# Kernel tuning notes

Measured on AMD Instinct MI355X. Metric: run time of the kernel, lower is better.

The kernel has to match this reference:

```python
import jax, jax.numpy as jnp
import numpy as np

REG_MAX = 16
NUM_CLASSES = 80
STRIDES = (8, 16, 32)
FEAT_SIZES = ((80, 80), (40, 40), (20, 20))
CLS_DIM = 256
REG_DIM = 256
B = 16


def setup_inputs() -> dict:
    key = jax.random.key(0)
    ks = jax.random.split(key, 32)
    inp = {}
    i = 0
    for l, (H, W) in enumerate(FEAT_SIZES):
        inp[f"cls_feat{l}"] = jax.random.normal(ks[i], (B, CLS_DIM, H, W), jnp.float32); i += 1
        inp[f"reg_feat{l}"] = jax.random.normal(ks[i], (B, REG_DIM, H, W), jnp.float32); i += 1
    bias_init = -float(np.log((1.0 - 0.01) / 0.01))
    for l in range(3):
        inp[f"obj_w{l}"] = jax.random.normal(ks[i], (1, REG_DIM), jnp.float32) * 0.02; i += 1
        inp[f"obj_b{l}"] = jnp.full((1,), bias_init, jnp.float32)
        inp[f"cls_w{l}"] = jax.random.normal(ks[i], (NUM_CLASSES, CLS_DIM), jnp.float32) * 0.02; i += 1
        inp[f"cls_b{l}"] = jnp.full((NUM_CLASSES,), bias_init, jnp.float32)
        inp[f"reg_w{l}"] = jax.random.normal(ks[i], (4 * REG_MAX, REG_DIM), jnp.float32) * 0.02; i += 1
        inp[f"reg_b{l}"] = jnp.ones((4 * REG_MAX,), jnp.float32)
    return inp


def _anchors(H, W, stride):
    ay, ax = jnp.meshgrid(jnp.arange(H, dtype=jnp.float32), jnp.arange(W, dtype=jnp.float32), indexing="ij")
    a = jnp.stack([ax, ay], axis=-1).reshape(-1, 2)  # [HW, 2] (x, y)
    return (a + 0.5) * stride


def _level(cls_feat, reg_feat, obj_w, obj_b, cls_w, cls_b, reg_w, reg_b, stride):
    Bb, _, H, W = cls_feat.shape
    M = H * W
    # 1x1 convs as channel contractions; output in [B, H, W, O] then flatten to [B, M, O]
    obj = (jnp.einsum("bchw,oc->bhwo", reg_feat, obj_w) + obj_b).reshape(Bb, M, 1)
    cls = (jnp.einsum("bchw,oc->bhwo", cls_feat, cls_w) + cls_b).reshape(Bb, M, NUM_CLASSES)
    reg = (jnp.einsum("bchw,oc->bhwo", reg_feat, reg_w) + reg_b).reshape(Bb, M, 4 * REG_MAX)
    # DFL decode: softmax over bins, expectation with proj = linspace(0, reg_max, reg_max)
    proj = jnp.linspace(0.0, float(REG_MAX), REG_MAX)
    dist = jax.nn.softmax(reg.reshape(Bb, M, 4, REG_MAX), axis=-1)
    reg_d = jnp.einsum("bmfr,r->bmf", dist, proj)  # [B, M, 4] (l, t, r, b)
    anchors = _anchors(H, W, stride)  # [M, 2]
    x1y1 = anchors[None] - reg_d[..., :2] * stride
    x2y2 = anchors[None] + reg_d[..., 2:] * stride
    box = jnp.concatenate([x1y1, x2y2], axis=-1)  # [B, M, 4]
    return jnp.concatenate([obj, cls, reg, box], axis=-1)  # [B, M, 1+80+64+4]


def reference(cls_feat0, cls_feat1, cls_feat2, reg_feat0, reg_feat1, reg_feat2,
              obj_w0, obj_b0, cls_w0, cls_b0, reg_w0, reg_b0,
              obj_w1, obj_b1, cls_w1, cls_b1, reg_w1, reg_b1,
              obj_w2, obj_b2, cls_w2, cls_b2, reg_w2, reg_b2):
    lvl0 = _level(cls_feat0, reg_feat0, obj_w0, obj_b0, cls_w0, cls_b0, reg_w0, reg_b0, STRIDES[0])
    lvl1 = _level(cls_feat1, reg_feat1, obj_w1, obj_b1, cls_w1, cls_b1, reg_w1, reg_b1, STRIDES[1])
    lvl2 = _level(cls_feat2, reg_feat2, obj_w2, obj_b2, cls_w2, cls_b2, reg_w2, reg_b2, STRIDES[2])
    # concat anchors along M: [B, 8400, 149]
    return jnp.concatenate([lvl0, lvl1, lvl2], axis=1)
```

## Files before the change

kernel.cpp:

```cpp
#include <hip/hip_runtime.h>
#include <stdint.h>

typedef __attribute__((ext_vector_type(4))) float f32x4;
typedef __attribute__((ext_vector_type(8))) short s16x8;

struct Params {
  const float* cls_feat[3];
  const float* reg_feat[3];
  const float* obj_w[3];
  const float* obj_b[3];
  const float* cls_w[3];
  const float* cls_b[3];
  const float* reg_w[3];
  const float* reg_b[3];
  float* out;
};

__device__ __forceinline__ unsigned short f2bf(float f) {
  unsigned int u = __builtin_bit_cast(unsigned int, f);
  u = (u + 0x7FFFu + ((u >> 16) & 1u)) >> 16;
  return (unsigned short)u;
}

__global__ __launch_bounds__(320, 5) void head_kernel(Params p) {
  const int tid  = threadIdx.x;
  const int lane = tid & 63;
  const int wave = tid >> 6;
  const int quad = lane >> 4;
  const int col  = lane & 15;
  const bool is_cls = (blockIdx.y == 0);

  int bx = blockIdx.x;
  int b  = bx / 105;
  int t  = bx - b * 105;
  int level, tloc;
  if (t < 80)       { level = 0; tloc = t; }
  else if (t < 100) { level = 1; tloc = t - 80; }
  else              { level = 2; tloc = t - 100; }

  const int   LW_[3]   = {80, 40, 20};
  const int   LM_[3]   = {6400, 1600, 400};
  const float LS_[3]   = {8.f, 16.f, 32.f};
  const int   LOFF_[3] = {0, 6400, 8000};

  const int   Mlvl = LM_[level];
  const int   Moff = LOFF_[level];
  const float strd = LS_[level];
  const int   m0   = tloc * 80;

  __shared__ __align__(16) short lds_feat[80 * 256];

  const f32x4 vzero = {0.f, 0.f, 0.f, 0.f};

  const int orow = wave * 16 + col;
  const float* wptr;
  if (is_cls)          wptr = p.cls_w[level] + orow * 256;
  else if (orow < 64)  wptr = p.reg_w[level] + orow * 256;
  else if (orow == 64) wptr = p.obj_w[level];
  else                 wptr = nullptr;

  f32x4 wv[16];
  #pragma unroll
  for (int s = 0; s < 8; ++s) {
    if (wptr) {
      const f32x4* wp = (const f32x4*)(wptr + s * 32 + quad * 8);
      wv[2 * s]     = wp[0];
      wv[2 * s + 1] = wp[1];
    } else {
      wv[2 * s]     = vzero;
      wv[2 * s + 1] = vzero;
    }
  }

  f32x4 bias = vzero;
  {
    const int o0 = wave * 16 + quad * 4;
    if (is_cls)        bias = *(const f32x4*)(p.cls_b[level] + o0);
    else if (o0 < 64)  bias = *(const f32x4*)(p.reg_b[level] + o0);
    else if (o0 == 64) bias[0] = p.obj_b[level][0];
  }

  const int mloc = tid % 80;
  const int cb0  = tid / 80;
  const float* featp = (is_cls ? p.cls_feat[level] : p.reg_feat[level])
                       + (size_t)b * 256 * (size_t)Mlvl + m0 + mloc;

  float f[2][8];
  #pragma unroll
  for (int j = 0; j < 8; ++j) f[0][j] = featp[(size_t)(cb0 * 8 + j) * Mlvl];

  s16x8 afrag[8];
  #pragma unroll
  for (int s = 0; s < 8; ++s) {
    s16x8 a;
    #pragma unroll
    for (int j = 0; j < 4; ++j) {
      a[j]     = (short)f2bf(wv[2 * s][j]);
      a[4 + j] = (short)f2bf(wv[2 * s + 1][j]);
    }
    afrag[s] = a;
  }

  const int swz = mloc & 7;
  #pragma unroll
  for (int i = 0; i < 8; ++i) {
    if (i < 7) {
      const int cbn = cb0 + 4 * (i + 1);
      #pragma unroll
      for (int j = 0; j < 8; ++j)
        f[(i + 1) & 1][j] = featp[(size_t)(cbn * 8 + j) * Mlvl];
    }
    const int cb = cb0 + 4 * i;
    s16x8 h;
    #pragma unroll
    for (int j = 0; j < 8; ++j) h[j] = (short)f2bf(f[i & 1][j]);
    *(s16x8*)&lds_feat[mloc * 256 + ((cb ^ swz) << 3)] = h;
  }

  __syncthreads();

  f32x4 acc[5];
  #pragma unroll
  for (int mf = 0; mf < 5; ++mf) acc[mf] = vzero;
  #pragma unroll
  for (int mf = 0; mf < 5; ++mf) {
    const int row = mf * 16 + col;
    const short* base = &lds_feat[row * 256];
    const int rswz = row & 7;
    #pragma unroll
    for (int s = 0; s < 8; ++s) {
      s16x8 bfrag = *(const s16x8*)(base + (((s * 4 + quad) ^ rswz) << 3));
      acc[mf] = __builtin_amdgcn_mfma_f32_16x16x32_bf16(afrag[s], bfrag, acc[mf], 0, 0, 0);
    }
  }

  const size_t outbase = (size_t)b * 8400 + Moff + m0;
  float* out = p.out;

  if (is_cls) {
    #pragma unroll
    for (int mf = 0; mf < 5; ++mf) {
      const int m = mf * 16 + col;
      f32x4 v = acc[mf] + bias;
      float* dst = out + (outbase + m) * 149 + 1 + wave * 16 + quad * 4;
      __builtin_memcpy(dst, &v, 16);
    }
    return;
  }

  float* g_lds = (float*)lds_feat;
  __syncthreads();

  if (wave < 4) {
    const float projscale = 16.f / 15.f;
    #pragma unroll
    for (int mf = 0; mf < 5; ++mf) {
      const int m = mf * 16 + col;
      f32x4 v = acc[mf] + bias;
      float* dst = out + (outbase + m) * 149 + 81 + wave * 16 + quad * 4;
      __builtin_memcpy(dst, &v, 16);
      float mx = fmaxf(fmaxf(v[0], v[1]), fmaxf(v[2], v[3]));
      mx = fmaxf(mx, __shfl_xor(mx, 16, 64));
      mx = fmaxf(mx, __shfl_xor(mx, 32, 64));
      const float e0 = __expf(v[0] - mx), e1 = __expf(v[1] - mx);
      const float e2 = __expf(v[2] - mx), e3 = __expf(v[3] - mx);
      float sden = e0 + e1 + e2 + e3;
      const float q4 = (float)(quad * 4);
      float n = q4 * e0 + (q4 + 1.f) * e1 + (q4 + 2.f) * e2 + (q4 + 3.f) * e3;
      sden += __shfl_xor(sden, 16, 64); sden += __shfl_xor(sden, 32, 64);
      n    += __shfl_xor(n, 16, 64);    n    += __shfl_xor(n, 32, 64);
      if (quad == 0) g_lds[wave * 80 + m] = projscale * n / sden;
    }
  } else {
    #pragma unroll
    for (int mf = 0; mf < 5; ++mf) {
      const int m = mf * 16 + col;
      if (quad == 0) out[(outbase + m) * 149] = acc[mf][0] + bias[0];
    }
  }

  __syncthreads();

  if (wave == 4) {
    #pragma unroll
    for (int it = 0; it < 2; ++it) {
      const int m = it * 64 + lane;
      if (m < 80) {
        const float g0 = g_lds[m], g1 = g_lds[80 + m];
        const float g2 = g_lds[160 + m], g3 = g_lds[240 + m];
        const int mg = m0 + m;
        int hh;
        if (level == 0)      hh = mg / 80;
        else if (level == 1) hh = mg / 40;
        else                 hh = mg / 20;
        const int ww = mg - hh * LW_[level];
        const float ax = (ww + 0.5f) * strd;
        const float ay = (hh + 0.5f) * strd;
        f32x4 bv;
        bv[0] = ax - g0 * strd; bv[1] = ay - g1 * strd;
        bv[2] = ax + g2 * strd; bv[3] = ay + g3 * strd;
        float* dst = out + (outbase + m) * 149 + 145;
        __builtin_memcpy(dst, &bv, 16);
      }
    }
  }
}

extern "C" void kernel_launch(void* const* d_in, const int* in_sizes, int n_in,
                              void* d_out, int out_size, void* d_ws, size_t ws_size,
                              hipStream_t stream) {
  (void)in_sizes; (void)n_in; (void)out_size; (void)d_ws; (void)ws_size;
  Params p;
  p.cls_feat[0] = (const float*)d_in[0];
  p.reg_feat[0] = (const float*)d_in[1];
  p.cls_feat[1] = (const float*)d_in[2];
  p.reg_feat[1] = (const float*)d_in[3];
  p.cls_feat[2] = (const float*)d_in[4];
  p.reg_feat[2] = (const float*)d_in[5];
  for (int l = 0; l < 3; ++l) {
    const int base = 6 + l * 6;
    p.obj_w[l] = (const float*)d_in[base + 0];
    p.obj_b[l] = (const float*)d_in[base + 1];
    p.cls_w[l] = (const float*)d_in[base + 2];
    p.cls_b[l] = (const float*)d_in[base + 3];
    p.reg_w[l] = (const float*)d_in[base + 4];
    p.reg_b[l] = (const float*)d_in[base + 5];
  }
  p.out = (float*)d_out;

  dim3 grid(16 * 105, 2);
  dim3 block(320);
  hipLaunchKernelGGL(head_kernel, grid, block, 0, stream, p);
}
```

Measured before the change: 358.7 us.

## Load feature tiles as float4 vectors and interleave weight/feature staging

Feature loading changes from scalar per-channel loads (one spatial position per thread) to 16-byte vector loads covering four spatial positions across four channels per thread. The values are transposed into LDS with a new XOR swizzle key to avoid bank conflicts. Weight loads and bf16 conversion are software-pipelined alongside the feature staging so global latency overlaps conversion work. The intent is to cut global load instruction count and improve coalescing, in exchange for more live registers and narrower 8-byte LDS writes.

```diff
diff --git a/kernel.cpp b/kernel.cpp
--- a/kernel.cpp
+++ b/kernel.cpp
@@ -3,6 +3,7 @@
 
 typedef __attribute__((ext_vector_type(4))) float f32x4;
 typedef __attribute__((ext_vector_type(8))) short s16x8;
+typedef __attribute__((ext_vector_type(4))) short s16x4;
 
 struct Params {
   const float* cls_feat[3];
@@ -22,6 +23,30 @@
   return (unsigned short)u;
 }
 
+__device__ __forceinline__ s16x8 cvt8(f32x4 a, f32x4 b, bool valid) {
+  s16x8 r;
+  #pragma unroll
+  for (int j = 0; j < 4; ++j) {
+    r[j]     = valid ? (short)f2bf(a[j]) : (short)0;
+    r[4 + j] = valid ? (short)f2bf(b[j]) : (short)0;
+  }
+  return r;
+}
+
+__device__ __forceinline__ void stage4(short* lds, int mq, int tq, int i,
+                                       f32x4 L0, f32x4 L1, f32x4 L2, f32x4 L3) {
+  #pragma unroll
+  for (int j = 0; j < 4; ++j) {
+    const int m   = mq * 4 + j;
+    const int key = ((m >> 2) ^ m) & 7;
+    const int swc = (tq >> 1) ^ key;
+    s16x4 h;
+    h[0] = (short)f2bf(L0[j]); h[1] = (short)f2bf(L1[j]);
+    h[2] = (short)f2bf(L2[j]); h[3] = (short)f2bf(L3[j]);
+    *(s16x4*)&lds[m * 256 + i * 64 + swc * 8 + (tq & 1) * 4] = h;
+  }
+}
+
 __global__ __launch_bounds__(320, 5) void head_kernel(Params p) {
   const int tid  = threadIdx.x;
   const int lane = tid & 63;
@@ -39,9 +64,9 @@
   else              { level = 2; tloc = t - 100; }
 
   const int   LW_[3]   = {80, 40, 20};
-  const int   LM_[3]   = {6400, 1600, 400};
   const float LS_[3]   = {8.f, 16.f, 32.f};
   const int   LOFF_[3] = {0, 6400, 8000};
+  const int   LM_[3]   = {6400, 1600, 400};
 
   const int   Mlvl = LM_[level];
   const int   Moff = LOFF_[level];
@@ -51,6 +76,12 @@
   __shared__ __align__(16) short lds_feat[80 * 256];
 
   const f32x4 vzero = {0.f, 0.f, 0.f, 0.f};
+
+  const int tq = tid / 20;
+  const int mq = tid - tq * 20;
+
+  const float* featp = (is_cls ? p.cls_feat[level] : p.reg_feat[level])
+                       + (size_t)b * 256 * (size_t)Mlvl + m0 + mq * 4;
 
   const int orow = wave * 16 + col;
   const float* wptr;
@@ -58,19 +89,19 @@
   else if (orow < 64)  wptr = p.reg_w[level] + orow * 256;
   else if (orow == 64) wptr = p.obj_w[level];
   else                 wptr = nullptr;
-
-  f32x4 wv[16];
-  #pragma unroll
-  for (int s = 0; s < 8; ++s) {
-    if (wptr) {
-      const f32x4* wp = (const f32x4*)(wptr + s * 32 + quad * 8);
-      wv[2 * s]     = wp[0];
-      wv[2 * s + 1] = wp[1];
-    } else {
-      wv[2 * s]     = vzero;
-      wv[2 * s + 1] = vzero;
-    }
-  }
+  const bool  wvalid = (wptr != nullptr);
+  const float* wq    = (wvalid ? wptr : p.obj_w[level]) + quad * 8;
+
+  #define WLD(s, h) (*(const f32x4*)(wq + (s) * 32 + (h) * 4))
+  #define FLD(i, c) (*(const f32x4*)(featp + (size_t)((i) * 64 + tq * 4 + (c)) * (size_t)Mlvl))
+
+  s16x8 afrag[8];
+  f32x4 wa, wb, wc, wd;
+  f32x4 A0, A1, A2, A3, B0, B1, B2, B3;
+
+  wa = WLD(0, 0); wb = WLD(0, 1); wc = WLD(1, 0); wd = WLD(1, 1);
+  A0 = FLD(0, 0); A1 = FLD(0, 1); A2 = FLD(0, 2); A3 = FLD(0, 3);
+  B0 = FLD(1, 0); B1 = FLD(1, 1); B2 = FLD(1, 2); B3 = FLD(1, 3);
 
   f32x4 bias = vzero;
   {
@@ -80,42 +111,19 @@
     else if (o0 == 64) bias[0] = p.obj_b[level][0];
   }
 
-  const int mloc = tid % 80;
-  const int cb0  = tid / 80;
-  const float* featp = (is_cls ? p.cls_feat[level] : p.reg_feat[level])
-                       + (size_t)b * 256 * (size_t)Mlvl + m0 + mloc;
-
-  float f[2][8];
-  #pragma unroll
-  for (int j = 0; j < 8; ++j) f[0][j] = featp[(size_t)(cb0 * 8 + j) * Mlvl];
-
-  s16x8 afrag[8];
-  #pragma unroll
-  for (int s = 0; s < 8; ++s) {
-    s16x8 a;
-    #pragma unroll
-    for (int j = 0; j < 4; ++j) {
-      a[j]     = (short)f2bf(wv[2 * s][j]);
-      a[4 + j] = (short)f2bf(wv[2 * s + 1][j]);
-    }
-    afrag[s] = a;
-  }
-
-  const int swz = mloc & 7;
-  #pragma unroll
-  for (int i = 0; i < 8; ++i) {
-    if (i < 7) {
-      const int cbn = cb0 + 4 * (i + 1);
-      #pragma unroll
-      for (int j = 0; j < 8; ++j)
-        f[(i + 1) & 1][j] = featp[(size_t)(cbn * 8 + j) * Mlvl];
-    }
-    const int cb = cb0 + 4 * i;
-    s16x8 h;
-    #pragma unroll
-    for (int j = 0; j < 8; ++j) h[j] = (short)f2bf(f[i & 1][j]);
-    *(s16x8*)&lds_feat[mloc * 256 + ((cb ^ swz) << 3)] = h;
-  }
+  afrag[0] = cvt8(wa, wb, wvalid); afrag[1] = cvt8(wc, wd, wvalid);
+  wa = WLD(2, 0); wb = WLD(2, 1); wc = WLD(3, 0); wd = WLD(3, 1);
+  stage4(lds_feat, mq, tq, 0, A0, A1, A2, A3);
+  A0 = FLD(2, 0); A1 = FLD(2, 1); A2 = FLD(2, 2); A3 = FLD(2, 3);
+  afrag[2] = cvt8(wa, wb, wvalid); afrag[3] = cvt8(wc, wd, wvalid);
+  wa = WLD(4, 0); wb = WLD(4, 1); wc = WLD(5, 0); wd = WLD(5, 1);
+  stage4(lds_feat, mq, tq, 1, B0, B1, B2, B3);
+  B0 = FLD(3, 0); B1 = FLD(3, 1); B2 = FLD(3, 2); B3 = FLD(3, 3);
+  afrag[4] = cvt8(wa, wb, wvalid); afrag[5] = cvt8(wc, wd, wvalid);
+  wa = WLD(6, 0); wb = WLD(6, 1); wc = WLD(7, 0); wd = WLD(7, 1);
+  stage4(lds_feat, mq, tq, 2, A0, A1, A2, A3);
+  afrag[6] = cvt8(wa, wb, wvalid); afrag[7] = cvt8(wc, wd, wvalid);
+  stage4(lds_feat, mq, tq, 3, B0, B1, B2, B3);
 
   __syncthreads();
 
@@ -124,12 +132,14 @@
   for (int mf = 0; mf < 5; ++mf) acc[mf] = vzero;
   #pragma unroll
   for (int mf = 0; mf < 5; ++mf) {
-    const int row = mf * 16 + col;
+    const int row  = mf * 16 + col;
+    const int rkey = ((row >> 2) ^ row) & 7;
     const short* base = &lds_feat[row * 256];
-    const int rswz = row & 7;
     #pragma unroll
     for (int s = 0; s < 8; ++s) {
-      s16x8 bfrag = *(const s16x8*)(base + (((s * 4 + quad) ^ rswz) << 3));
+      const int c16 = 4 * s + quad;
+      const int sw  = (c16 & ~7) | ((c16 & 7) ^ rkey);
+      s16x8 bfrag = *(const s16x8*)(base + sw * 8);
       acc[mf] = __builtin_amdgcn_mfma_f32_16x16x32_bf16(afrag[s], bfrag, acc[mf], 0, 0, 0);
     }
   }
```

Measured after the change: 359.2 us. About the same (+0.1%).

## Stage features via global_load_lds with 64-anchor tiles and fused cls/reg phases

Applied to the files above, without the earlier changes.

Each block now handles 64 anchors instead of 80 and processes both the cls and the reg/obj branch in sequence, replacing the two-block-per-tile grid. Feature channels are loaded with direct global-to-LDS loads into an fp32 tile in two 128-channel halves, using a rotated layout. The bf16 conversion now happens when the B fragments are read back from LDS. The aim is to cut register-staged loads and launch overhead and to improve load issue. In exchange the LDS reads become scalar strided loads with conversion inside the MFMA loop, and each block adds extra syncs.

```diff
diff --git a/kernel.cpp b/kernel.cpp
--- a/kernel.cpp
+++ b/kernel.cpp
@@ -22,172 +22,172 @@
   return (unsigned short)u;
 }
 
+__device__ __forceinline__ s16x8 cvt8(f32x4 a, f32x4 b, bool ok) {
+  s16x8 r;
+  #pragma unroll
+  for (int j = 0; j < 4; ++j) {
+    r[j]     = ok ? (short)f2bf(a[j]) : (short)0;
+    r[4 + j] = ok ? (short)f2bf(b[j]) : (short)0;
+  }
+  return r;
+}
+
+__device__ __forceinline__ void gload_lds4(const float* g, float* l) {
+  __builtin_amdgcn_global_load_lds(
+      (const __attribute__((address_space(1))) unsigned int*)g,
+      (__attribute__((address_space(3))) unsigned int*)l, 4, 0, 0);
+}
+
 __global__ __launch_bounds__(320, 5) void head_kernel(Params p) {
   const int tid  = threadIdx.x;
   const int lane = tid & 63;
   const int wave = tid >> 6;
   const int quad = lane >> 4;
   const int col  = lane & 15;
-  const bool is_cls = (blockIdx.y == 0);
 
   int bx = blockIdx.x;
-  int b  = bx / 105;
-  int t  = bx - b * 105;
+  int b  = bx / 132;
+  int t  = bx - b * 132;
   int level, tloc;
-  if (t < 80)       { level = 0; tloc = t; }
-  else if (t < 100) { level = 1; tloc = t - 80; }
-  else              { level = 2; tloc = t - 100; }
+  if (t < 100)      { level = 0; tloc = t; }
+  else if (t < 125) { level = 1; tloc = t - 100; }
+  else              { level = 2; tloc = t - 125; }
 
   const int   LW_[3]   = {80, 40, 20};
-  const int   LM_[3]   = {6400, 1600, 400};
   const float LS_[3]   = {8.f, 16.f, 32.f};
   const int   LOFF_[3] = {0, 6400, 8000};
+  const int   LM_[3]   = {6400, 1600, 400};
 
   const int   Mlvl = LM_[level];
   const int   Moff = LOFF_[level];
   const float strd = LS_[level];
-  const int   m0   = tloc * 80;
-
-  __shared__ __align__(16) short lds_feat[80 * 256];
-
-  const f32x4 vzero = {0.f, 0.f, 0.f, 0.f};
-
-  const int orow = wave * 16 + col;
-  const float* wptr;
-  if (is_cls)          wptr = p.cls_w[level] + orow * 256;
-  else if (orow < 64)  wptr = p.reg_w[level] + orow * 256;
-  else if (orow == 64) wptr = p.obj_w[level];
-  else                 wptr = nullptr;
-
-  f32x4 wv[16];
-  #pragma unroll
-  for (int s = 0; s < 8; ++s) {
-    if (wptr) {
-      const f32x4* wp = (const f32x4*)(wptr + s * 32 + quad * 8);
-      wv[2 * s]     = wp[0];
-      wv[2 * s + 1] = wp[1];
-    } else {
-      wv[2 * s]     = vzero;
-      wv[2 * s + 1] = vzero;
-    }
-  }
-
-  f32x4 bias = vzero;
-  {
-    const int o0 = wave * 16 + quad * 4;
+  const int   m0   = tloc * 64;
+  int valid = Mlvl - m0; if (valid > 64) valid = 64;
+
+  __shared__ __align__(16) float lds_f[128 * 64];
+
+  const size_t outbase = (size_t)b * 8400 + Moff + m0;
+  float* out = p.out;
+  const int orow    = wave * 16 + col;
+  const int o0      = wave * 16 + quad * 4;
+  const int rotbase = col + quad * 8;
+
+  for (int ph = 0; ph < 2; ++ph) {
+    const bool is_cls = (ph == 0);
+    const float* featp = (is_cls ? p.cls_feat[level] : p.reg_feat[level])
+                         + (size_t)b * 256 * (size_t)Mlvl + m0;
+
+    const float* wptr;
+    bool wvalid = true;
+    if (is_cls)          wptr = p.cls_w[level] + orow * 256;
+    else if (orow < 64)  wptr = p.reg_w[level] + orow * 256;
+    else if (orow == 64) wptr = p.obj_w[level];
+    else               { wptr = p.obj_w[level]; wvalid = false; }
+    const float* wq = wptr + quad * 8;
+
+    f32x4 bias = {0.f, 0.f, 0.f, 0.f};
     if (is_cls)        bias = *(const f32x4*)(p.cls_b[level] + o0);
     else if (o0 < 64)  bias = *(const f32x4*)(p.reg_b[level] + o0);
     else if (o0 == 64) bias[0] = p.obj_b[level][0];
-  }
-
-  const int mloc = tid % 80;
-  const int cb0  = tid / 80;
-  const float* featp = (is_cls ? p.cls_feat[level] : p.reg_feat[level])
-                       + (size_t)b * 256 * (size_t)Mlvl + m0 + mloc;
-
-  float f[2][8];
-  #pragma unroll
-  for (int j = 0; j < 8; ++j) f[0][j] = featp[(size_t)(cb0 * 8 + j) * Mlvl];
-
-  s16x8 afrag[8];
-  #pragma unroll
-  for (int s = 0; s < 8; ++s) {
-    s16x8 a;
+
+    f32x4 acc[4];
     #pragma unroll
-    for (int j = 0; j < 4; ++j) {
-      a[j]     = (short)f2bf(wv[2 * s][j]);
-      a[4 + j] = (short)f2bf(wv[2 * s + 1][j]);
+    for (int mf = 0; mf < 4; ++mf) acc[mf] = (f32x4){0.f, 0.f, 0.f, 0.f};
+
+    #pragma unroll
+    for (int h = 0; h < 2; ++h) {
+      __syncthreads();
+
+      const float* wqh = wq + h * 128;
+      f32x4 w0a = *(const f32x4*)(wqh + 0);
+      f32x4 w0b = *(const f32x4*)(wqh + 4);
+      f32x4 w1a = *(const f32x4*)(wqh + 32);
+      f32x4 w1b = *(const f32x4*)(wqh + 36);
+
+      for (int r = wave; r < 128; r += 5) {
+        const int rot = ((r >> 3) & 3) << 3;
+        int mi = (lane - rot) & 63;
+        if (mi >= valid) mi = valid - 1;
+        gload_lds4(featp + (size_t)(h * 128 + r) * (size_t)Mlvl + mi,
+                   &lds_f[r * 64]);
+      }
+
+      s16x8 af0 = cvt8(w0a, w0b, wvalid);
+      s16x8 af1 = cvt8(w1a, w1b, wvalid);
+      f32x4 w2a = *(const f32x4*)(wqh + 64);
+      f32x4 w2b = *(const f32x4*)(wqh + 68);
+      f32x4 w3a = *(const f32x4*)(wqh + 96);
+      f32x4 w3b = *(const f32x4*)(wqh + 100);
+
+      __syncthreads();
+
+      s16x8 af2 = cvt8(w2a, w2b, wvalid);
+      s16x8 af3 = cvt8(w3a, w3b, wvalid);
+      s16x8 afr[4] = {af0, af1, af2, af3};
+
+      #pragma unroll
+      for (int mf = 0; mf < 4; ++mf) {
+        const int rotm = (rotbase + mf * 16) & 63;
+        #pragma unroll
+        for (int s = 0; s < 4; ++s) {
+          const float* bp = &lds_f[(s * 32 + quad * 8) * 64 + rotm];
+          s16x8 bf;
+          #pragma unroll
+          for (int j = 0; j < 8; ++j) bf[j] = (short)f2bf(bp[j * 64]);
+          acc[mf] = __builtin_amdgcn_mfma_f32_16x16x32_bf16(afr[s], bf, acc[mf], 0, 0, 0);
+        }
+      }
     }
-    afrag[s] = a;
-  }
-
-  const int swz = mloc & 7;
-  #pragma unroll
-  for (int i = 0; i < 8; ++i) {
-    if (i < 7) {
-      const int cbn = cb0 + 4 * (i + 1);
+
+    if (is_cls) {
       #pragma unroll
-      for (int j = 0; j < 8; ++j)
-        f[(i + 1) & 1][j] = featp[(size_t)(cbn * 8 + j) * Mlvl];
-    }
-    const int cb = cb0 + 4 * i;
-    s16x8 h;
-    #pragma unroll
-    for (int j = 0; j < 8; ++j) h[j] = (short)f2bf(f[i & 1][j]);
-    *(s16x8*)&lds_feat[mloc * 256 + ((cb ^ swz) << 3)] = h;
-  }
-
-  __syncthreads();
-
-  f32x4 acc[5];
-  #pragma unroll
-  for (int mf = 0; mf < 5; ++mf) acc[mf] = vzero;
-  #pragma unroll
-  for (int mf = 0; mf < 5; ++mf) {
-    const int row = mf * 16 + col;
-    const short* base = &lds_feat[row * 256];
-    const int rswz = row & 7;
-    #pragma unroll
-    for (int s = 0; s < 8; ++s) {
-      s16x8 bfrag = *(const s16x8*)(base + (((s * 4 + quad) ^ rswz) << 3));
-      acc[mf] = __builtin_amdgcn_mfma_f32_16x16x32_bf16(afrag[s], bfrag, acc[mf], 0, 0, 0);
-    }
-  }
-
-  const size_t outbase = (size_t)b * 8400 + Moff + m0;
-  float* out = p.out;
-
-  if (is_cls) {
-    #pragma unroll
-    for (int mf = 0; mf < 5; ++mf) {
-      const int m = mf * 16 + col;
-      f32x4 v = acc[mf] + bias;
-      float* dst = out + (outbase + m) * 149 + 1 + wave * 16 + quad * 4;
-      __builtin_memcpy(dst, &v, 16);
-    }
-    return;
-  }
-
-  float* g_lds = (float*)lds_feat;
-  __syncthreads();
-
-  if (wave < 4) {
-    const float projscale = 16.f / 15.f;
-    #pragma unroll
-    for (int mf = 0; mf < 5; ++mf) {
-      const int m = mf * 16 + col;
-      f32x4 v = acc[mf] + bias;
-      float* dst = out + (outbase + m) * 149 + 81 + wave * 16 + quad * 4;
-      __builtin_memcpy(dst, &v, 16);
-      float mx = fmaxf(fmaxf(v[0], v[1]), fmaxf(v[2], v[3]));
-      mx = fmaxf(mx, __shfl_xor(mx, 16, 64));
-      mx = fmaxf(mx, __shfl_xor(mx, 32, 64));
-      const float e0 = __expf(v[0] - mx), e1 = __expf(v[1] - mx);
-      const float e2 = __expf(v[2] - mx), e3 = __expf(v[3] - mx);
-      float sden = e0 + e1 + e2 + e3;
-      const float q4 = (float)(quad * 4);
-      float n = q4 * e0 + (q4 + 1.f) * e1 + (q4 + 2.f) * e2 + (q4 + 3.f) * e3;
-      sden += __shfl_xor(sden, 16, 64); sden += __shfl_xor(sden, 32, 64);
-      n    += __shfl_xor(n, 16, 64);    n    += __shfl_xor(n, 32, 64);
-      if (quad == 0) g_lds[wave * 80 + m] = projscale * n / sden;
-    }
-  } else {
-    #pragma unroll
-    for (int mf = 0; mf < 5; ++mf) {
-      const int m = mf * 16 + col;
-      if (quad == 0) out[(outbase + m) * 149] = acc[mf][0] + bias[0];
-    }
-  }
-
-  __syncthreads();
-
-  if (wave == 4) {
-    #pragma unroll
-    for (int it = 0; it < 2; ++it) {
-      const int m = it * 64 + lane;
-      if (m < 80) {
-        const float g0 = g_lds[m], g1 = g_lds[80 + m];
-        const float g2 = g_lds[160 + m], g3 = g_lds[240 + m];
+      for (int mf = 0; mf < 4; ++mf) {
+        const int m = mf * 16 + col;
+        if (m < valid) {
+          f32x4 v = acc[mf] + bias;
+          float* dst = out + (outbase + m) * 149 + 1 + wave * 16 + quad * 4;
+          __builtin_memcpy(dst, &v, 16);
+        }
+      }
+    } else {
+      __syncthreads();
+      float* g_lds = lds_f;
+      if (wave < 4) {
+        const float projscale = 16.f / 15.f;
+        #pragma unroll
+        for (int mf = 0; mf < 4; ++mf) {
+          const int m = mf * 16 + col;
+          f32x4 v = acc[mf] + bias;
+          if (m < valid) {
+            float* dst = out + (outbase + m) * 149 + 81 + wave * 16 + quad * 4;
+            __builtin_memcpy(dst, &v, 16);
+          }
+          float mx = fmaxf(fmaxf(v[0], v[1]), fmaxf(v[2], v[3]));
+          mx = fmaxf(mx, __shfl_xor(mx, 16, 64));
+          mx = fmaxf(mx, __shfl_xor(mx, 32, 64));
+          const float e0 = __expf(v[0] - mx), e1 = __expf(v[1] - mx);
+          const float e2 = __expf(v[2] - mx), e3 = __expf(v[3] - mx);
+          float sden = e0 + e1 + e2 + e3;
+          const float q4 = (float)(quad * 4);
+          float n = q4 * e0 + (q4 + 1.f) * e1 + (q4 + 2.f) * e2 + (q4 + 3.f) * e3;
+          sden += __shfl_xor(sden, 16, 64); sden += __shfl_xor(sden, 32, 64);
+          n    += __shfl_xor(n, 16, 64);    n    += __shfl_xor(n, 32, 64);
+          if (quad == 0) g_lds[wave * 64 + m] = projscale * n / sden;
+        }
+      } else {
+        #pragma unroll
+        for (int mf = 0; mf < 4; ++mf) {
+          const int m = mf * 16 + col;
+          if (quad == 0 && m < valid)
+            out[(outbase + m) * 149] = acc[mf][0] + bias[0];
+        }
+      }
+      __syncthreads();
+
+      if (wave == 4 && lane < valid) {
+        const int m = lane;
+        const float g0 = g_lds[m],       g1 = g_lds[64 + m];
+        const float g2 = g_lds[128 + m], g3 = g_lds[192 + m];
         const int mg = m0 + m;
         int hh;
         if (level == 0)      hh = mg / 80;
@@ -228,7 +228,7 @@
   }
   p.out = (float*)d_out;
 
-  dim3 grid(16 * 105, 2);
+  dim3 grid(16 * 132);
   dim3 block(320);
   hipLaunchKernelGGL(head_kernel, grid, block, 0, stream, p);
 }
```

After: 451.6 us. +25.9%, slower.
